# Performance work log

Hardware: AMD Instinct MI355X
Metric: run time of the kernel (lower is better)

The kernel has to match this reference:

```python
import jax, jax.numpy as jnp
import numpy as np

N = 50000          # neuron_count
NNZ = 1_600_000    # edges (avg degree 32)
B = 32             # batch
L = 3              # CONNECTOME_LAYER_NUMBER


def setup_inputs() -> dict:
    key = jax.random.key(0)
    k1, k2, k3, k4, k5 = jax.random.split(key, 5)
    x = jax.random.normal(k1, (B, N), dtype=jnp.float32)
    adj_vals = jax.random.uniform(k2, (NNZ,), dtype=jnp.float32)
    w_vals = jax.random.uniform(k3, (NNZ,), dtype=jnp.float32)
    bias = jnp.ones((N,), dtype=jnp.float32)
    row = jax.random.randint(k4, (NNZ,), 0, N, dtype=jnp.int32)
    col = jax.random.randint(k5, (NNZ,), 0, N, dtype=jnp.int32)
    return {"x": x, "adj_vals": adj_vals, "w_vals": w_vals, "bias": bias,
            "row": row, "col": col}


def _spmm(vals, row, col, dense, n):
    # (sparse NxN) @ dense [N, B] via gather + segment_sum scatter
    contrib = vals[:, None] * dense[col]          # [nnz, B]
    return jax.ops.segment_sum(contrib, row, num_segments=n)


def reference(x, adj_vals, w_vals, bias, row, col):
    # Original per layer: x = ((A @ W) @ x^T)^T + bias.
    # We use associativity: (A @ W) @ x^T == A @ (W @ x^T), avoiding the
    # explicit SpGEMM while computing the same linear map.
    n = bias.shape[0]
    xt = x.T                                      # [N, B]
    for _ in range(L):
        wx = _spmm(w_vals, row, col, xt, n)       # W @ x^T -> [N, B]
        xt = _spmm(adj_vals, row, col, wx, n)     # A @ (W @ x^T)
        xt = xt + bias[:, None]                   # broadcast bias over batch
    return xt.T                                   # [B, N]
```

## Files before the change

kernel.cpp:

```cpp
#include <hip/hip_runtime.h>


#define NN 50000
#define NNZ_E 1600000
#define NB (NN * 32)
#define CHUNK 3072
#define NBLK1 ((NNZ_E + CHUNK - 1) / CHUNK)
#define NBIN ((NN + 127) / 128)
#define NH (NBIN * NBLK1)
#define CAP2 5120
#define BCAP 6144
#define LENP (NBIN * BCAP)
#define SCAN_NBLK ((NH + 255) / 256)
#define TIN_BLKS 98

__device__ __forceinline__ int clampi(int v, int hi) {
    v = v < 0 ? 0 : v;
    return v > hi ? hi : v;
}

__device__ __forceinline__ unsigned short f2h(float v) {
    union { _Float16 h; unsigned short u; } cv;
    cv.h = (_Float16)v;
    return cv.u;
}

__device__ __forceinline__ float kv_val(unsigned kv) {
    union { unsigned short u; _Float16 h; } cv;
    cv.u = (unsigned short)(kv >> 16);
    return (float)cv.h;
}

__global__ __launch_bounds__(256) void hist_kernel(const int* __restrict__ row,
                                                   int* __restrict__ hist1,
                                                   const float* __restrict__ x,
                                                   _Float16* __restrict__ xt) {
    __shared__ int h[NBIN];
    int blk = blockIdx.x, tid = threadIdx.x;
    if (blk >= NBLK1) {
        for (int i = (blk - NBLK1) * 256 + tid; i < NB; i += TIN_BLKS * 256) {
            int n = i >> 5;
            int b = i & 31;
            xt[i] = (_Float16)x[b * NN + n];
        }
        return;
    }
    for (int j = tid; j < NBIN; j += 256) h[j] = 0;
    __syncthreads();
    int base = blk * CHUNK;
    int n = NNZ_E - base; if (n > CHUNK) n = CHUNK;
    for (int i = tid; i < n; i += 256)
        atomicAdd(&h[clampi(row[base + i], NN - 1) >> 7], 1);
    __syncthreads();
    for (int j = tid; j < NBIN; j += 256) hist1[j * NBLK1 + blk] = h[j];
}

__global__ void scan_local_kernel(int* __restrict__ data, int n, int* __restrict__ bsum) {
    __shared__ int s[256];
    int i = blockIdx.x * 256 + threadIdx.x;
    int v = (i < n) ? data[i] : 0;
    s[threadIdx.x] = v;
    __syncthreads();
    for (int off = 1; off < 256; off <<= 1) {
        int t = (threadIdx.x >= off) ? s[threadIdx.x - off] : 0;
        __syncthreads();
        s[threadIdx.x] += t;
        __syncthreads();
    }
    if (i < n) data[i] = s[threadIdx.x] - v;
    if (threadIdx.x == 255) bsum[blockIdx.x] = s[threadIdx.x];
}

__global__ __launch_bounds__(256) void scanfin_kernel(int* __restrict__ data, int n,
                                                      const int* __restrict__ bsum, int m,
                                                      int* __restrict__ binstart) {
    __shared__ int sa[1024];
    __shared__ int sb[1024];
    int tid = threadIdx.x;
#pragma unroll
    for (int q = 0; q < 4; ++q) {
        int p = tid + q * 256;
        sa[p] = (p < m) ? bsum[p] : 0;
    }
    __syncthreads();
    int* src = sa;
    int* dst = sb;
    for (int off = 1; off < 1024; off <<= 1) {
#pragma unroll
        for (int q = 0; q < 4; ++q) {
            int p = tid + q * 256;
            int v = src[p];
            if (p >= off) v += src[p - off];
            dst[p] = v;
        }
        __syncthreads();
        int* t = src; src = dst; dst = t;
    }
    int add = (blockIdx.x > 0) ? src[blockIdx.x - 1] : 0;
    int i = blockIdx.x * 256 + tid;
    if (i < n) {
        int v = data[i] + add;
        data[i] = v;
        if (i % NBLK1 == 0) binstart[i / NBLK1] = v;
    }
    if (i == 0) binstart[NBIN] = NNZ_E;
}

__global__ __launch_bounds__(256) void pass1_kernel(
        const int* __restrict__ row, const int* __restrict__ col,
        const float* __restrict__ a, const float* __restrict__ w,
        const int* __restrict__ hist1_off,
        uint2* __restrict__ e1) {
    __shared__ int h[NBIN];
    __shared__ int hscan[NBIN];
    __shared__ int hoff[NBIN];
    __shared__ int s256[256];
    __shared__ unsigned sKey[CHUNK];
    __shared__ unsigned sAW[CHUNK];
    int blk = blockIdx.x, tid = threadIdx.x;
    int base = blk * CHUNK;
    int n = NNZ_E - base; if (n > CHUNK) n = CHUNK;

    for (int j = tid; j < NBIN; j += 256) {
        h[j] = 0;
        hoff[j] = hist1_off[j * NBLK1 + blk];
    }
    __syncthreads();
    for (int i = tid; i < n; i += 256)
        atomicAdd(&h[clampi(row[base + i], NN - 1) >> 7], 1);
    __syncthreads();
    int j0 = tid * 2, j1 = tid * 2 + 1;
    int c0 = (j0 < NBIN) ? h[j0] : 0;
    int c1 = (j1 < NBIN) ? h[j1] : 0;
    int tsum = c0 + c1;
    s256[tid] = tsum;
    __syncthreads();
    for (int off = 1; off < 256; off <<= 1) {
        int t = (tid >= off) ? s256[tid - off] : 0;
        __syncthreads();
        s256[tid] += t;
        __syncthreads();
    }
    int ex = s256[tid] - tsum;
    __syncthreads();
    if (j0 < NBIN) { hscan[j0] = ex;      h[j0] = ex; }
    if (j1 < NBIN) { hscan[j1] = ex + c0; h[j1] = ex + c0; }
    __syncthreads();
    for (int i = tid; i < n; i += 256) {
        int r = clampi(row[base + i], NN - 1);
        int c = clampi(col[base + i], NN - 1);
        int bin = r >> 7;
        int p = atomicAdd(&h[bin], 1);
        p = clampi(p, n - 1);
        sKey[p] = ((unsigned)r << 16) | (unsigned)c;
        sAW[p] = ((unsigned)f2h(a[base + i]) << 16) | (unsigned)f2h(w[base + i]);
    }
    __syncthreads();
    for (int p = tid; p < n; p += 256) {
        unsigned key = sKey[p];
        int bin = (int)(key >> 23);
        int d = clampi(hoff[bin] + (p - hscan[bin]), NNZ_E - 1);
        e1[d] = make_uint2(key, sAW[p]);
    }
}

__global__ __launch_bounds__(256) void pass2_kernel(
        const uint2* __restrict__ e1, const int* __restrict__ binstart,
        unsigned* __restrict__ kvA2, unsigned* __restrict__ kvW2,
        unsigned* __restrict__ row_desc) {
    __shared__ int rh[128];
    __shared__ int rs[128];
    __shared__ int cur[128];
    int bin = blockIdx.x, tid = threadIdx.x;
    int r0 = bin << 7;
    int rows = NN - r0; if (rows > 128) rows = 128;
    int base = clampi(binstart[bin], NNZ_E);
    int size = clampi(binstart[bin + 1], NNZ_E) - base;
    size = clampi(size, CAP2);
    int pbase = bin * BCAP;

    if (tid < 128) rh[tid] = 0;
    __syncthreads();
    for (int i = tid; i < size; i += 256)
        atomicAdd(&rh[(e1[base + i].x >> 16) & 127], 1);
    __syncthreads();
    int cnt  = (tid < 128) ? rh[tid] : 0;
    int plen = (cnt + 7) & ~7;
    if (tid < 128) rs[tid] = plen;
    __syncthreads();
    for (int off = 1; off < 128; off <<= 1) {
        int t = (tid >= off && tid < 128) ? rs[tid - off] : 0;
        __syncthreads();
        if (tid < 128) rs[tid] += t;
        __syncthreads();
    }
    int rofs = (tid < 128) ? clampi(rs[tid] - plen, BCAP - 8) : 0;
    if (tid < 128) cur[tid] = rofs;
    if (tid < rows)
        row_desc[r0 + tid] = (unsigned)(pbase + rofs) | ((unsigned)(plen >> 3) << 24);
    __syncthreads();
    for (int i = tid; i < size; i += 256) {
        uint2 e = e1[base + i];
        unsigned key = e.x;
        unsigned aw  = e.y;
        int rl = (key >> 16) & 127;
        int p = atomicAdd(&cur[rl], 1);
        p = clampi(p, BCAP - 1);
        unsigned c = key & 0xFFFFu;
        kvA2[pbase + p] = (aw & 0xFFFF0000u) | c;
        kvW2[pbase + p] = (aw << 16) | c;
    }
    __syncthreads();
    if (tid < rows) {
        int pl = (rh[tid] + 7) & ~7;
        for (int q = rh[tid]; q < pl; ++q) {
            int d = clampi(rofs + q, BCAP - 1);
            kvA2[pbase + d] = 0u;
            kvW2[pbase + d] = 0u;
        }
    }
}

template <int WITH_BIAS, int FINAL>
__global__ __launch_bounds__(256) void spmm_kernel(
        const uint2* __restrict__ kv2, const unsigned* __restrict__ row_desc,
        const unsigned* __restrict__ in32, unsigned* __restrict__ out32,
        const float* __restrict__ bias, float outScale, float biasScale,
        float* __restrict__ outf) {
    int t = blockIdx.x * 256 + threadIdx.x;
    int r = t >> 4;
    int l = t & 15;
    if (r >= NN) return;
    unsigned d = row_desc[r];
    int niter = (int)(d >> 24);
    int base2 = clampi((int)(d & 0xFFFFFFu), LENP - 8) >> 1;
    float accL = 0.0f, accH = 0.0f;
    uint2 k2[4];
    if (niter > 0) {
#pragma unroll
        for (int q = 0; q < 4; ++q) k2[q] = kv2[base2 + q];
    }
    for (int it = 0; it < niter; ++it) {
        unsigned k[8];
#pragma unroll
        for (int q = 0; q < 4; ++q) { k[2 * q] = k2[q].x; k[2 * q + 1] = k2[q].y; }
        unsigned gd[8];
#pragma unroll
        for (int j = 0; j < 8; ++j) gd[j] = in32[((k[j] & 0xFFFFu) << 4) + l];
        if (it + 1 < niter) {
            int nb2 = base2 + (it + 1) * 4;
#pragma unroll
            for (int q = 0; q < 4; ++q) k2[q] = kv2[nb2 + q];
        }
#pragma unroll
        for (int j = 0; j < 8; ++j) {
            float v = kv_val(k[j]);
            union { unsigned u; _Float16 h[2]; } cv;
            cv.u = gd[j];
            accL += v * (float)cv.h[0];
            accH += v * (float)cv.h[1];
        }
    }
    float rL = accL * outScale, rH = accH * outScale;
    if (WITH_BIAS) {
        float bb = bias[r] * biasScale;
        rL += bb; rH += bb;
    }
    if (FINAL) {
        outf[(2 * l) * NN + r]     = rL * 16777216.0f;
        outf[(2 * l + 1) * NN + r] = rH * 16777216.0f;
    } else {
        union { unsigned u; _Float16 h[2]; } o;
        o.h[0] = (_Float16)rL;
        o.h[1] = (_Float16)rH;
        out32[(r << 4) + l] = o.u;
    }
}

extern "C" void kernel_launch(void* const* d_in, const int* in_sizes, int n_in,
                              void* d_out, int out_size, void* d_ws, size_t ws_size,
                              hipStream_t stream) {
    const float* x        = (const float*)d_in[0];
    const float* adj_vals = (const float*)d_in[1];
    const float* w_vals   = (const float*)d_in[2];
    const float* bias     = (const float*)d_in[3];
    const int*   row      = (const int*)d_in[4];
    const int*   col      = (const int*)d_in[5];
    float* out = (float*)d_out;

    uint2*     e1        = (uint2*)d_ws;
    unsigned*  kvA2      = (unsigned*)(e1 + NNZ_E);
    unsigned*  kvW2      = kvA2 + LENP;
    _Float16*  xt16      = (_Float16*)(kvW2 + LENP);
    _Float16*  tmp16     = xt16 + NB;
    int*   hist1         = (int*)(tmp16 + NB);
    int*   bsumB         = hist1 + NH;
    int*   binstart      = bsumB + 1024;
    unsigned* row_desc   = (unsigned*)(binstart + NBIN + 8);

    const int BS = 256;
    const int grid_spmm = (NN * 16 + BS - 1) / BS;

    hist_kernel<<<NBLK1 + TIN_BLKS, BS, 0, stream>>>(row, hist1, x, xt16);
    scan_local_kernel<<<SCAN_NBLK, BS, 0, stream>>>(hist1, NH, bsumB);
    scanfin_kernel<<<SCAN_NBLK, BS, 0, stream>>>(hist1, NH, bsumB, SCAN_NBLK, binstart);

    pass1_kernel<<<NBLK1, BS, 0, stream>>>(row, col, adj_vals, w_vals,
                                           hist1, e1);
    pass2_kernel<<<NBIN, BS, 0, stream>>>(e1, binstart, kvA2, kvW2, row_desc);

    const uint2* kvA = (const uint2*)kvA2;
    const uint2* kvW = (const uint2*)kvW2;
    const unsigned* xt32  = (const unsigned*)xt16;
    unsigned*       xt32w = (unsigned*)xt16;
    const unsigned* tm32  = (const unsigned*)tmp16;
    unsigned*       tm32w = (unsigned*)tmp16;

    const float r256 = 1.0f / 256.0f;
    spmm_kernel<0, 0><<<grid_spmm, BS, 0, stream>>>(kvW, row_desc, xt32, tm32w,
                                                    nullptr, 1.0f, 0.0f, nullptr);
    spmm_kernel<1, 0><<<grid_spmm, BS, 0, stream>>>(kvA, row_desc, tm32, xt32w,
                                                    bias, r256, 1.0f / 256.0f, nullptr);
    spmm_kernel<0, 0><<<grid_spmm, BS, 0, stream>>>(kvW, row_desc, xt32, tm32w,
                                                    nullptr, 1.0f, 0.0f, nullptr);
    spmm_kernel<1, 0><<<grid_spmm, BS, 0, stream>>>(kvA, row_desc, tm32, xt32w,
                                                    bias, r256, 1.0f / 65536.0f, nullptr);
    spmm_kernel<0, 0><<<grid_spmm, BS, 0, stream>>>(kvW, row_desc, xt32, tm32w,
                                                    nullptr, 1.0f, 0.0f, nullptr);
    spmm_kernel<1, 1><<<grid_spmm, BS, 0, stream>>>(kvA, row_desc, tm32, xt32w,
                                                    bias, r256, 1.0f / 16777216.0f, out);
}
```

Baseline: 246.2 us.

## Replace histogram-scan preprocessing with atomic per-bin cursors and fixed-capacity bins

The separate histogram kernel and the two-level global prefix scan are removed. pass1 now claims each block's range within a bin with a global atomicAdd on a per-bin cursor and writes edges into fixed-capacity bin slots. The x transpose moves into extra blocks of pass1. This cuts three kernel launches and a full read of row, but edge order inside a bin now depends on atomic timing, which makes fp16 accumulation order nondeterministic. Bins over capacity are clamped.

```diff
diff --git a/kernel.cpp b/kernel.cpp
--- a/kernel.cpp
+++ b/kernel.cpp
@@ -7,11 +7,11 @@
 #define CHUNK 3072
 #define NBLK1 ((NNZ_E + CHUNK - 1) / CHUNK)
 #define NBIN ((NN + 127) / 128)
-#define NH (NBIN * NBLK1)
 #define CAP2 5120
+#define BCAP1 6144
+#define LENE (NBIN * BCAP1)
 #define BCAP 6144
 #define LENP (NBIN * BCAP)
-#define SCAN_NBLK ((NH + 255) / 256)
 #define TIN_BLKS 98
 
 __device__ __forceinline__ int clampi(int v, int hi) {
@@ -31,86 +31,11 @@
     return (float)cv.h;
 }
 
-__global__ __launch_bounds__(256) void hist_kernel(const int* __restrict__ row,
-                                                   int* __restrict__ hist1,
-                                                   const float* __restrict__ x,
-                                                   _Float16* __restrict__ xt) {
-    __shared__ int h[NBIN];
-    int blk = blockIdx.x, tid = threadIdx.x;
-    if (blk >= NBLK1) {
-        for (int i = (blk - NBLK1) * 256 + tid; i < NB; i += TIN_BLKS * 256) {
-            int n = i >> 5;
-            int b = i & 31;
-            xt[i] = (_Float16)x[b * NN + n];
-        }
-        return;
-    }
-    for (int j = tid; j < NBIN; j += 256) h[j] = 0;
-    __syncthreads();
-    int base = blk * CHUNK;
-    int n = NNZ_E - base; if (n > CHUNK) n = CHUNK;
-    for (int i = tid; i < n; i += 256)
-        atomicAdd(&h[clampi(row[base + i], NN - 1) >> 7], 1);
-    __syncthreads();
-    for (int j = tid; j < NBIN; j += 256) hist1[j * NBLK1 + blk] = h[j];
-}
-
-__global__ void scan_local_kernel(int* __restrict__ data, int n, int* __restrict__ bsum) {
-    __shared__ int s[256];
-    int i = blockIdx.x * 256 + threadIdx.x;
-    int v = (i < n) ? data[i] : 0;
-    s[threadIdx.x] = v;
-    __syncthreads();
-    for (int off = 1; off < 256; off <<= 1) {
-        int t = (threadIdx.x >= off) ? s[threadIdx.x - off] : 0;
-        __syncthreads();
-        s[threadIdx.x] += t;
-        __syncthreads();
-    }
-    if (i < n) data[i] = s[threadIdx.x] - v;
-    if (threadIdx.x == 255) bsum[blockIdx.x] = s[threadIdx.x];
-}
-
-__global__ __launch_bounds__(256) void scanfin_kernel(int* __restrict__ data, int n,
-                                                      const int* __restrict__ bsum, int m,
-                                                      int* __restrict__ binstart) {
-    __shared__ int sa[1024];
-    __shared__ int sb[1024];
-    int tid = threadIdx.x;
-#pragma unroll
-    for (int q = 0; q < 4; ++q) {
-        int p = tid + q * 256;
-        sa[p] = (p < m) ? bsum[p] : 0;
-    }
-    __syncthreads();
-    int* src = sa;
-    int* dst = sb;
-    for (int off = 1; off < 1024; off <<= 1) {
-#pragma unroll
-        for (int q = 0; q < 4; ++q) {
-            int p = tid + q * 256;
-            int v = src[p];
-            if (p >= off) v += src[p - off];
-            dst[p] = v;
-        }
-        __syncthreads();
-        int* t = src; src = dst; dst = t;
-    }
-    int add = (blockIdx.x > 0) ? src[blockIdx.x - 1] : 0;
-    int i = blockIdx.x * 256 + tid;
-    if (i < n) {
-        int v = data[i] + add;
-        data[i] = v;
-        if (i % NBLK1 == 0) binstart[i / NBLK1] = v;
-    }
-    if (i == 0) binstart[NBIN] = NNZ_E;
-}
-
 __global__ __launch_bounds__(256) void pass1_kernel(
         const int* __restrict__ row, const int* __restrict__ col,
         const float* __restrict__ a, const float* __restrict__ w,
-        const int* __restrict__ hist1_off,
-        uint2* __restrict__ e1) {
+        int* __restrict__ cursor, uint2* __restrict__ e1,
+        const float* __restrict__ x, _Float16* __restrict__ xt) {
     __shared__ int h[NBIN];
     __shared__ int hscan[NBIN];
     __shared__ int hoff[NBIN];
@@ -118,13 +43,18 @@
     __shared__ unsigned sKey[CHUNK];
     __shared__ unsigned sAW[CHUNK];
     int blk = blockIdx.x, tid = threadIdx.x;
+    if (blk >= NBLK1) {
+        for (int i = (blk - NBLK1) * 256 + tid; i < NB; i += TIN_BLKS * 256) {
+            int n = i >> 5;
+            int b = i & 31;
+            xt[i] = (_Float16)x[b * NN + n];
+        }
+        return;
+    }
     int base = blk * CHUNK;
     int n = NNZ_E - base; if (n > CHUNK) n = CHUNK;
 
-    for (int j = tid; j < NBIN; j += 256) {
-        h[j] = 0;
-        hoff[j] = hist1_off[j * NBLK1 + blk];
-    }
+    for (int j = tid; j < NBIN; j += 256) h[j] = 0;
     __syncthreads();
     for (int i = tid; i < n; i += 256)
         atomicAdd(&h[clampi(row[base + i], NN - 1) >> 7], 1);
@@ -143,8 +73,18 @@
     }
     int ex = s256[tid] - tsum;
     __syncthreads();
-    if (j0 < NBIN) { hscan[j0] = ex;      h[j0] = ex; }
-    if (j1 < NBIN) { hscan[j1] = ex + c0; h[j1] = ex + c0; }
+    if (j0 < NBIN) {
+        hscan[j0] = ex;
+        h[j0] = ex;
+        int b0 = c0 ? atomicAdd(&cursor[j0], c0) : 0;
+        hoff[j0] = j0 * BCAP1 + clampi(b0, BCAP1 - 1);
+    }
+    if (j1 < NBIN) {
+        hscan[j1] = ex + c0;
+        h[j1] = ex + c0;
+        int b1 = c1 ? atomicAdd(&cursor[j1], c1) : 0;
+        hoff[j1] = j1 * BCAP1 + clampi(b1, BCAP1 - 1);
+    }
     __syncthreads();
     for (int i = tid; i < n; i += 256) {
         int r = clampi(row[base + i], NN - 1);
@@ -159,13 +99,13 @@
     for (int p = tid; p < n; p += 256) {
         unsigned key = sKey[p];
         int bin = (int)(key >> 23);
-        int d = clampi(hoff[bin] + (p - hscan[bin]), NNZ_E - 1);
+        int d = clampi(hoff[bin] + (p - hscan[bin]), LENE - 1);
         e1[d] = make_uint2(key, sAW[p]);
     }
 }
 
 __global__ __launch_bounds__(256) void pass2_kernel(
-        const uint2* __restrict__ e1, const int* __restrict__ binstart,
+        const uint2* __restrict__ e1, const int* __restrict__ cursor,
         unsigned* __restrict__ kvA2, unsigned* __restrict__ kvW2,
         unsigned* __restrict__ row_desc) {
     __shared__ int rh[128];
@@ -174,15 +114,14 @@
     int bin = blockIdx.x, tid = threadIdx.x;
     int r0 = bin << 7;
     int rows = NN - r0; if (rows > 128) rows = 128;
-    int base = clampi(binstart[bin], NNZ_E);
-    int size = clampi(binstart[bin + 1], NNZ_E) - base;
-    size = clampi(size, CAP2);
+    int ebase = bin * BCAP1;
+    int size = clampi(cursor[bin], CAP2);
     int pbase = bin * BCAP;
 
     if (tid < 128) rh[tid] = 0;
     __syncthreads();
     for (int i = tid; i < size; i += 256)
-        atomicAdd(&rh[(e1[base + i].x >> 16) & 127], 1);
+        atomicAdd(&rh[(e1[ebase + i].x >> 16) & 127], 1);
     __syncthreads();
     int cnt  = (tid < 128) ? rh[tid] : 0;
     int plen = (cnt + 7) & ~7;
@@ -200,7 +139,7 @@
         row_desc[r0 + tid] = (unsigned)(pbase + rofs) | ((unsigned)(plen >> 3) << 24);
     __syncthreads();
     for (int i = tid; i < size; i += 256) {
-        uint2 e = e1[base + i];
+        uint2 e = e1[ebase + i];
         unsigned key = e.x;
         unsigned aw  = e.y;
         int rl = (key >> 16) & 127;
@@ -289,25 +228,20 @@
     float* out = (float*)d_out;
 
     uint2*     e1        = (uint2*)d_ws;
-    unsigned*  kvA2      = (unsigned*)(e1 + NNZ_E);
+    unsigned*  kvA2      = (unsigned*)(e1 + LENE);
     unsigned*  kvW2      = kvA2 + LENP;
     _Float16*  xt16      = (_Float16*)(kvW2 + LENP);
     _Float16*  tmp16     = xt16 + NB;
-    int*   hist1         = (int*)(tmp16 + NB);
-    int*   bsumB         = hist1 + NH;
-    int*   binstart      = bsumB + 1024;
-    unsigned* row_desc   = (unsigned*)(binstart + NBIN + 8);
+    int*       cursor    = (int*)(tmp16 + NB);
+    unsigned*  row_desc  = (unsigned*)(cursor + NBIN + 8);
 
     const int BS = 256;
     const int grid_spmm = (NN * 16 + BS - 1) / BS;
 
-    hist_kernel<<<NBLK1 + TIN_BLKS, BS, 0, stream>>>(row, hist1, x, xt16);
-    scan_local_kernel<<<SCAN_NBLK, BS, 0, stream>>>(hist1, NH, bsumB);
-    scanfin_kernel<<<SCAN_NBLK, BS, 0, stream>>>(hist1, NH, bsumB, SCAN_NBLK, binstart);
-
-    pass1_kernel<<<NBLK1, BS, 0, stream>>>(row, col, adj_vals, w_vals,
-                                           hist1, e1);
-    pass2_kernel<<<NBIN, BS, 0, stream>>>(e1, binstart, kvA2, kvW2, row_desc);
+    hipMemsetAsync(cursor, 0, NBIN * sizeof(int), stream);
+    pass1_kernel<<<NBLK1 + TIN_BLKS, BS, 0, stream>>>(row, col, adj_vals, w_vals,
+                                                      cursor, e1, x, xt16);
+    pass2_kernel<<<NBIN, BS, 0, stream>>>(e1, cursor, kvA2, kvW2, row_desc);
 
     const uint2* kvA = (const uint2*)kvA2;
     const uint2* kvW = (const uint2*)kvW2;
```

Result: faster. 235.6 us (-4.3%).
